# Performance work log

Measured on AMD Instinct MI355X. Metric: run time of the kernel, lower is better.

## Reference

```python
import jax, jax.numpy as jnp
import numpy as np

EPS = 1e-5
B, CIN, COUT, H, W = 32, 512, 512, 56, 56
K = 4            # kernel_num
A = 32           # attention_channel = max(int(512*0.0625), 16)


def setup_inputs() -> dict:
    key = jax.random.key(0)
    ks = jax.random.split(key, 16)
    s = lambda fan: 1.0 / np.sqrt(fan)
    return {
        "x": jax.random.normal(ks[0], (B, CIN, H, W), jnp.float32),
        # attention trunk: global-avgpool -> fc -> bn -> relu
        "fc_w": jax.random.normal(ks[1], (A, CIN), jnp.float32) * s(CIN),
        "abn_g": jnp.ones((A,), jnp.float32),
        "abn_b": jnp.zeros((A,), jnp.float32),
        "abn_m": jax.random.normal(ks[2], (A,), jnp.float32) * 0.1,
        "abn_v": jax.random.uniform(ks[3], (A,), jnp.float32, 0.5, 1.5),
        # channel / filter / kernel attention heads
        "ch_w": jax.random.normal(ks[4], (CIN, A), jnp.float32) * s(A),
        "ch_b": jnp.zeros((CIN,), jnp.float32),
        "fl_w": jax.random.normal(ks[5], (COUT, A), jnp.float32) * s(A),
        "fl_b": jnp.zeros((COUT,), jnp.float32),
        "kn_w": jax.random.normal(ks[6], (K, A), jnp.float32) * s(A),
        "kn_b": jnp.zeros((K,), jnp.float32),
        # base 1x1 conv weight bank [kernel_num, out, in] (1x1 spatial squeezed)
        "weight": jax.random.normal(ks[7], (K, COUT, CIN), jnp.float32) * s(CIN),
        # output BatchNorm2d (eval mode: running stats)
        "bn_g": jnp.ones((COUT,), jnp.float32),
        "bn_b": jnp.zeros((COUT,), jnp.float32),
        "bn_m": jax.random.normal(ks[8], (COUT,), jnp.float32) * 0.1,
        "bn_v": jax.random.uniform(ks[9], (COUT,), jnp.float32, 0.5, 1.5),
    }


def reference(x, fc_w, abn_g, abn_b, abn_m, abn_v,
              ch_w, ch_b, fl_w, fl_b, kn_w, kn_b,
              weight, bn_g, bn_b, bn_m, bn_v):
    # ---- omni-dimensional attention (kernel_size=1 => spatial attn skipped) ----
    pooled = jnp.mean(x, axis=(2, 3))                       # [B, Cin]
    h = pooled @ fc_w.T                                     # [B, A]
    h = (h - abn_m) * (abn_g / jnp.sqrt(abn_v + EPS)) + abn_b
    h = jax.nn.relu(h)
    ch_att = jax.nn.sigmoid(h @ ch_w.T + ch_b)              # [B, Cin]
    fl_att = jax.nn.sigmoid(h @ fl_w.T + fl_b)              # [B, Cout]
    kn_att = jax.nn.softmax(h @ kn_w.T + kn_b, axis=1)      # [B, K] (temperature=1)
    # ---- per-sample aggregated 1x1 kernel + grouped(batch) pointwise conv ----
    agg_w = jnp.einsum('bk,koc->boc', kn_att, weight)       # [B, Cout, Cin]
    xm = x * ch_att[:, :, None, None]                       # channel attention
    y = jnp.einsum('bchw,boc->bohw', xm, agg_w)             # batched 1x1 conv
    y = y * fl_att[:, :, None, None]                        # filter attention
    # ---- BatchNorm2d (inference) ----
    inv = bn_g / jnp.sqrt(bn_v + EPS)
    y = (y - bn_m[None, :, None, None]) * inv[None, :, None, None] + bn_b[None, :, None, None]
    return y
```

## Files before the change

### kernel.cpp

```cpp
#include <hip/hip_runtime.h>
#include <math.h>

#define BATCH 32
#define CIN   512
#define COUT  512
#define HW    3136
#define KNUM  4
#define ADIM  32
#define EPS   1e-5f

static constexpr size_t XT_OFF     = 0;
static constexpr size_t WF_OFF     = 102760448;
static constexpr size_t POOLED_OFF = 119537664;
static constexpr size_t H_OFF      = 119603200;
static constexpr size_t CH_OFF     = 119607296;
static constexpr size_t FLINV_OFF  = 119672832;
static constexpr size_t KN_OFF     = 119738368;
static constexpr size_t BETA_OFF   = 119738880;

typedef __attribute__((ext_vector_type(8))) short short8;
typedef __attribute__((ext_vector_type(4))) float float4v;

typedef const unsigned int __attribute__((address_space(1)))* gas_ptr;
typedef unsigned int __attribute__((address_space(3)))* lds_ptr;

__device__ __forceinline__ unsigned short f2bf(float f) {
  unsigned int u = __float_as_uint(f);
  u += 0x7FFFu + ((u >> 16) & 1u);
  return (unsigned short)(u >> 16);
}

__global__ void zero_f32(float* __restrict__ p, int n) {
  int i = blockIdx.x * blockDim.x + threadIdx.x;
  if (i < n) p[i] = 0.f;
}

__global__ __launch_bounds__(256) void transpose_pool(
    const float* __restrict__ x, unsigned short* __restrict__ xT,
    float* __restrict__ pooled) {
  __shared__ unsigned short T[64 * 68];
  const int pb = blockIdx.x * 64;
  const int cb = blockIdx.y * 64;
  const int b  = blockIdx.z;
  const int t  = threadIdx.x;
  const int mp = t & 15;
  const int mc = t >> 4;
  const int c0 = cb + mc * 4;
  const int p0 = pb + mp * 4;

  const float* xp = x + (size_t)(b * CIN + c0) * HW + p0;
  float a[4][4];
  #pragma unroll
  for (int r = 0; r < 4; ++r) {
    float4 v = *(const float4*)(xp + (size_t)r * HW);
    a[r][0] = v.x; a[r][1] = v.y; a[r][2] = v.z; a[r][3] = v.w;
    float s = v.x + v.y + v.z + v.w;
    #pragma unroll
    for (int off = 8; off > 0; off >>= 1) s += __shfl_down(s, off, 16);
    if (mp == 0) atomicAdd(&pooled[b * CIN + c0 + r], s);
  }
  #pragma unroll
  for (int j = 0; j < 4; ++j) {
    ushort4 w;
    w.x = f2bf(a[0][j]); w.y = f2bf(a[1][j]);
    w.z = f2bf(a[2][j]); w.w = f2bf(a[3][j]);
    *(ushort4*)&T[(mp * 4 + j) * 68 + mc * 4] = w;
  }
  __syncthreads();
  const int pr = t >> 2, cp = t & 3;
  const int base = pr * 68 + cp * 16;
  uint2 r0 = *(uint2*)&T[base + 0];
  uint2 r1 = *(uint2*)&T[base + 4];
  uint2 r2 = *(uint2*)&T[base + 8];
  uint2 r3 = *(uint2*)&T[base + 12];
  unsigned short* dst = xT + (size_t)(b * HW + pb + pr) * CIN + cb + cp * 16;
  *(uint4*)(dst)     = make_uint4(r0.x, r0.y, r1.x, r1.y);
  *(uint4*)(dst + 8) = make_uint4(r2.x, r2.y, r3.x, r3.y);
}

__global__ __launch_bounds__(256) void attn_h_kn(
    const float* __restrict__ pooled, const float* __restrict__ fc_w,
    const float* __restrict__ abn_g, const float* __restrict__ abn_b,
    const float* __restrict__ abn_m, const float* __restrict__ abn_v,
    const float* __restrict__ kn_w, const float* __restrict__ kn_b,
    float* __restrict__ h_out, float* __restrict__ kn_out) {
  __shared__ float hs[ADIM];
  const int b = blockIdx.x, t = threadIdx.x;
  const int a = t >> 3, part = t & 7;
  const float* pr = pooled + b * CIN;
  const float* fr = fc_w + a * CIN;
  float s = 0.f;
  const int cb = part * 64;
  #pragma unroll 8
  for (int c = 0; c < 64; ++c) s += pr[cb + c] * fr[cb + c];
  #pragma unroll
  for (int off = 4; off > 0; off >>= 1) s += __shfl_down(s, off, 8);
  if (part == 0) {
    s *= (1.0f / (float)HW);
    float vv = (s - abn_m[a]) * (abn_g[a] * rsqrtf(abn_v[a] + EPS)) + abn_b[a];
    vv = fmaxf(vv, 0.f);
    hs[a] = vv;
    h_out[b * ADIM + a] = vv;
  }
  __syncthreads();
  if (t == 0) {
    float lg[KNUM]; float mx = -1e30f;
    for (int k = 0; k < KNUM; ++k) {
      float acc = kn_b[k];
      for (int aa = 0; aa < ADIM; ++aa) acc += hs[aa] * kn_w[k * ADIM + aa];
      lg[k] = acc; mx = fmaxf(mx, acc);
    }
    float ssum = 0.f;
    for (int k = 0; k < KNUM; ++k) { lg[k] = expf(lg[k] - mx); ssum += lg[k]; }
    for (int k = 0; k < KNUM; ++k) kn_out[b * KNUM + k] = lg[k] / ssum;
  }
}

__global__ void beta_kernel(const float* __restrict__ bn_g, const float* __restrict__ bn_b,
                            const float* __restrict__ bn_m, const float* __restrict__ bn_v,
                            float* __restrict__ beta) {
  int o = blockIdx.x * 256 + threadIdx.x;
  if (o < COUT) {
    float inv = bn_g[o] * rsqrtf(bn_v[o] + EPS);
    beta[o] = bn_b[o] - bn_m[o] * inv;
  }
}

__global__ __launch_bounds__(128) void attn_heads(
    const float* __restrict__ h, const float* __restrict__ ch_w, const float* __restrict__ ch_b,
    const float* __restrict__ fl_w, const float* __restrict__ fl_b,
    const float* __restrict__ bn_g, const float* __restrict__ bn_v,
    float* __restrict__ ch_out, float* __restrict__ flinv_out) {
  __shared__ float hs[ADIM];
  const int ck = blockIdx.x, b = blockIdx.y, t = threadIdx.x;
  if (t < ADIM) hs[t] = h[b * ADIM + t];
  __syncthreads();
  if (ck < 4) {
    int c = ck * 128 + t;
    const float* wr = ch_w + c * ADIM;
    float acc = ch_b[c];
    #pragma unroll
    for (int aa = 0; aa < ADIM; ++aa) acc += hs[aa] * wr[aa];
    ch_out[b * CIN + c] = 1.f / (1.f + expf(-acc));
  } else {
    int o = (ck - 4) * 128 + t;
    const float* wr = fl_w + o * ADIM;
    float acc = fl_b[o];
    #pragma unroll
    for (int aa = 0; aa < ADIM; ++aa) acc += hs[aa] * wr[aa];
    float sig = 1.f / (1.f + expf(-acc));
    flinv_out[b * COUT + o] = sig * (bn_g[o] * rsqrtf(bn_v[o] + EPS));
  }
}

__global__ __launch_bounds__(256) void build_wf(
    const float* __restrict__ weight, const float* __restrict__ kn,
    const float* __restrict__ ch, const float* __restrict__ flinv,
    unsigned short* __restrict__ Wf) {
  const int och = blockIdx.x, b = blockIdx.y, t = threadIdx.x;
  const int o0 = och * 16;
  const float k0 = kn[b * KNUM + 0], k1 = kn[b * KNUM + 1];
  const float k2 = kn[b * KNUM + 2], k3 = kn[b * KNUM + 3];
  #pragma unroll
  for (int i = 0; i < 8; ++i) {
    int cell = i * 1024 + t * 4;
    int ol = cell >> 9, c = cell & 511;
    int o = o0 + ol;
    float fi = flinv[b * COUT + o];
    const float* wp = weight + (size_t)o * CIN + c;
    float4 w0 = *(const float4*)(wp);
    float4 w1 = *(const float4*)(wp + 1 * CIN * COUT);
    float4 w2 = *(const float4*)(wp + 2 * CIN * COUT);
    float4 w3 = *(const float4*)(wp + 3 * CIN * COUT);
    float4 cv = *(const float4*)(ch + b * CIN + c);
    ushort4 r;
    r.x = f2bf((k0 * w0.x + k1 * w1.x + k2 * w2.x + k3 * w3.x) * cv.x * fi);
    r.y = f2bf((k0 * w0.y + k1 * w1.y + k2 * w2.y + k3 * w3.y) * cv.y * fi);
    r.z = f2bf((k0 * w0.z + k1 * w1.z + k2 * w2.z + k3 * w3.z) * cv.z * fi);
    r.w = f2bf((k0 * w0.w + k1 * w1.w + k2 * w2.w + k3 * w3.w) * cv.w * fi);
    *(ushort4*)(Wf + (size_t)(b * COUT + o) * CIN + c) = r;
  }
}

__global__ __launch_bounds__(256) void gemm_kernel(
    const unsigned short* __restrict__ xT, const unsigned short* __restrict__ Wf,
    const float* __restrict__ beta, float* __restrict__ y) {
  __shared__ unsigned short lA[128 * 32];
  __shared__ unsigned short lB[128 * 32];
  const int pt = blockIdx.x, ot = blockIdx.y, b = blockIdx.z;
  const int o0 = ot * 128, p0 = pt * 128;
  const int t = threadIdx.x;
  const int wave = t >> 6, lane = t & 63;
  const int wm = wave & 1, wn = wave >> 1;

  const int lrow = lane >> 2;
  const int lcol = (lane & 3) * 8;
  const int r0 = (wave * 2 + 0) * 16 + lrow;
  const int r1 = (wave * 2 + 1) * 16 + lrow;

  const unsigned short* Ab = Wf + (size_t)b * COUT * CIN;
  const unsigned short* Bb = xT + (size_t)b * HW * CIN;
  const unsigned short* agp0 = Ab + (size_t)(o0 + r0) * CIN + lcol;
  const unsigned short* agp1 = Ab + (size_t)(o0 + r1) * CIN + lcol;
  int bp0 = p0 + r0; if (bp0 > HW - 1) bp0 = HW - 1;
  int bp1 = p0 + r1; if (bp1 > HW - 1) bp1 = HW - 1;
  const unsigned short* bgp0 = Bb + (size_t)bp0 * CIN + lcol;
  const unsigned short* bgp1 = Bb + (size_t)bp1 * CIN + lcol;

  unsigned short* lA0 = &lA[(wave * 2 + 0) * 512];
  unsigned short* lA1 = &lA[(wave * 2 + 1) * 512];
  unsigned short* lB0 = &lB[(wave * 2 + 0) * 512];
  unsigned short* lB1 = &lB[(wave * 2 + 1) * 512];

  float4v acc[4][4];
  #pragma unroll
  for (int i = 0; i < 4; ++i)
    #pragma unroll
    for (int j = 0; j < 4; ++j)
      #pragma unroll
      for (int r = 0; r < 4; ++r) acc[i][j][r] = 0.f;

  const int arow = lane & 15;
  const int kofs = (lane >> 4) * 8;

  for (int kt = 0; kt < CIN / 32; ++kt) {
    const int c0 = kt * 32;
    __syncthreads();
    __builtin_amdgcn_global_load_lds((gas_ptr)(const void*)(agp0 + c0), (lds_ptr)(void*)lA0, 16, 0, 0);
    __builtin_amdgcn_global_load_lds((gas_ptr)(const void*)(agp1 + c0), (lds_ptr)(void*)lA1, 16, 0, 0);
    __builtin_amdgcn_global_load_lds((gas_ptr)(const void*)(bgp0 + c0), (lds_ptr)(void*)lB0, 16, 0, 0);
    __builtin_amdgcn_global_load_lds((gas_ptr)(const void*)(bgp1 + c0), (lds_ptr)(void*)lB1, 16, 0, 0);
    __syncthreads();

    short8 af[4], bfr[4];
    #pragma unroll
    for (int i = 0; i < 4; ++i)
      af[i] = *(const short8*)&lA[(wm * 64 + i * 16 + arow) * 32 + kofs];
    #pragma unroll
    for (int j = 0; j < 4; ++j)
      bfr[j] = *(const short8*)&lB[(wn * 64 + j * 16 + arow) * 32 + kofs];
    #pragma unroll
    for (int i = 0; i < 4; ++i)
      #pragma unroll
      for (int j = 0; j < 4; ++j)
        acc[i][j] = __builtin_amdgcn_mfma_f32_16x16x32_bf16(af[i], bfr[j], acc[i][j], 0, 0, 0);
  }

  const int rowq = (lane >> 4) * 4;
  const int coln = lane & 15;
  #pragma unroll
  for (int i = 0; i < 4; ++i) {
    const int obase = o0 + wm * 64 + i * 16 + rowq;
    float bet[4];
    #pragma unroll
    for (int r = 0; r < 4; ++r) bet[r] = beta[obase + r];
    #pragma unroll
    for (int j = 0; j < 4; ++j) {
      const int p = p0 + wn * 64 + j * 16 + coln;
      if (p < HW) {
        #pragma unroll
        for (int r = 0; r < 4; ++r)
          y[(size_t)(b * COUT + obase + r) * HW + p] = acc[i][j][r] + bet[r];
      }
    }
  }
}

extern "C" void kernel_launch(void* const* d_in, const int* in_sizes, int n_in,
                              void* d_out, int out_size, void* d_ws, size_t ws_size,
                              hipStream_t stream) {
  (void)in_sizes; (void)n_in; (void)out_size; (void)ws_size;
  const float* x     = (const float*)d_in[0];
  const float* fc_w  = (const float*)d_in[1];
  const float* abn_g = (const float*)d_in[2];
  const float* abn_b = (const float*)d_in[3];
  const float* abn_m = (const float*)d_in[4];
  const float* abn_v = (const float*)d_in[5];
  const float* ch_w  = (const float*)d_in[6];
  const float* ch_b  = (const float*)d_in[7];
  const float* fl_w  = (const float*)d_in[8];
  const float* fl_b  = (const float*)d_in[9];
  const float* kn_w  = (const float*)d_in[10];
  const float* kn_b  = (const float*)d_in[11];
  const float* weight= (const float*)d_in[12];
  const float* bn_g  = (const float*)d_in[13];
  const float* bn_b  = (const float*)d_in[14];
  const float* bn_m  = (const float*)d_in[15];
  const float* bn_v  = (const float*)d_in[16];
  float* out = (float*)d_out;

  char* ws = (char*)d_ws;
  unsigned short* xT   = (unsigned short*)(ws + XT_OFF);
  unsigned short* Wf   = (unsigned short*)(ws + WF_OFF);
  float* pooled = (float*)(ws + POOLED_OFF);
  float* h      = (float*)(ws + H_OFF);
  float* ch     = (float*)(ws + CH_OFF);
  float* flinv  = (float*)(ws + FLINV_OFF);
  float* kn     = (float*)(ws + KN_OFF);
  float* beta   = (float*)(ws + BETA_OFF);

  zero_f32<<<64, 256, 0, stream>>>(pooled, BATCH * CIN);
  transpose_pool<<<dim3(HW / 64, CIN / 64, BATCH), 256, 0, stream>>>(x, xT, pooled);
  attn_h_kn<<<BATCH, 256, 0, stream>>>(pooled, fc_w, abn_g, abn_b, abn_m, abn_v,
                                       kn_w, kn_b, h, kn);
  beta_kernel<<<2, 256, 0, stream>>>(bn_g, bn_b, bn_m, bn_v, beta);
  attn_heads<<<dim3(8, BATCH), 128, 0, stream>>>(h, ch_w, ch_b, fl_w, fl_b, bn_g, bn_v,
                                                 ch, flinv);
  build_wf<<<dim3(32, BATCH), 256, 0, stream>>>(weight, kn, ch, flinv, Wf);
  gemm_kernel<<<dim3(25, 4, BATCH), 256, 0, stream>>>(xT, Wf, beta, out);
}
```

Measured before the change: 501.8 us.

## Fuse attention kernels, drop atomics, widen GEMM K-tile with swizzled LDS

Pooling no longer uses atomicAdd plus a zeroing kernel. Each transpose block now handles 256 channels and writes per-block partial sums, which a single fused attention kernel reduces before computing h, kernel, channel and filter attention. The separate beta kernel is gone and the BN bias is computed in the GEMM epilogue. The GEMM K-tile doubles to 64 with an XOR-swizzled LDS layout to avoid bank conflicts, halving loop iterations and barriers, and the grid order changes so the o-tiles sharing an xT tile run adjacently. The costs are more LDS per block and less parallelism in the transpose kernel.

```diff
diff --git a/kernel.cpp b/kernel.cpp
--- a/kernel.cpp
+++ b/kernel.cpp
@@ -9,14 +9,12 @@
 #define ADIM  32
 #define EPS   1e-5f
 
-static constexpr size_t XT_OFF     = 0;
-static constexpr size_t WF_OFF     = 102760448;
-static constexpr size_t POOLED_OFF = 119537664;
-static constexpr size_t H_OFF      = 119603200;
-static constexpr size_t CH_OFF     = 119607296;
-static constexpr size_t FLINV_OFF  = 119672832;
-static constexpr size_t KN_OFF     = 119738368;
-static constexpr size_t BETA_OFF   = 119738880;
+static constexpr size_t XT_OFF    = 0;
+static constexpr size_t WF_OFF    = 102760448;
+static constexpr size_t PART_OFF  = 119537664;
+static constexpr size_t CH_OFF    = 122748928;
+static constexpr size_t FLINV_OFF = 122814464;
+static constexpr size_t KN_OFF    = 122880000;
 
 typedef __attribute__((ext_vector_type(8))) short short8;
 typedef __attribute__((ext_vector_type(4))) float float4v;
@@ -30,77 +28,89 @@
   return (unsigned short)(u >> 16);
 }
 
-__global__ void zero_f32(float* __restrict__ p, int n) {
-  int i = blockIdx.x * blockDim.x + threadIdx.x;
-  if (i < n) p[i] = 0.f;
-}
-
 __global__ __launch_bounds__(256) void transpose_pool(
     const float* __restrict__ x, unsigned short* __restrict__ xT,
-    float* __restrict__ pooled) {
+    float* __restrict__ part) {
   __shared__ unsigned short T[64 * 68];
-  const int pb = blockIdx.x * 64;
-  const int cb = blockIdx.y * 64;
-  const int b  = blockIdx.z;
+  const int pb    = blockIdx.x * 64;
+  const int cbase = blockIdx.y * 256;
+  const int b     = blockIdx.z;
   const int t  = threadIdx.x;
   const int mp = t & 15;
   const int mc = t >> 4;
-  const int c0 = cb + mc * 4;
   const int p0 = pb + mp * 4;
-
-  const float* xp = x + (size_t)(b * CIN + c0) * HW + p0;
-  float a[4][4];
-  #pragma unroll
-  for (int r = 0; r < 4; ++r) {
-    float4 v = *(const float4*)(xp + (size_t)r * HW);
-    a[r][0] = v.x; a[r][1] = v.y; a[r][2] = v.z; a[r][3] = v.w;
-    float s = v.x + v.y + v.z + v.w;
-    #pragma unroll
-    for (int off = 8; off > 0; off >>= 1) s += __shfl_down(s, off, 16);
-    if (mp == 0) atomicAdd(&pooled[b * CIN + c0 + r], s);
-  }
-  #pragma unroll
-  for (int j = 0; j < 4; ++j) {
-    ushort4 w;
-    w.x = f2bf(a[0][j]); w.y = f2bf(a[1][j]);
-    w.z = f2bf(a[2][j]); w.w = f2bf(a[3][j]);
-    *(ushort4*)&T[(mp * 4 + j) * 68 + mc * 4] = w;
-  }
-  __syncthreads();
   const int pr = t >> 2, cp = t & 3;
-  const int base = pr * 68 + cp * 16;
-  uint2 r0 = *(uint2*)&T[base + 0];
-  uint2 r1 = *(uint2*)&T[base + 4];
-  uint2 r2 = *(uint2*)&T[base + 8];
-  uint2 r3 = *(uint2*)&T[base + 12];
-  unsigned short* dst = xT + (size_t)(b * HW + pb + pr) * CIN + cb + cp * 16;
-  *(uint4*)(dst)     = make_uint4(r0.x, r0.y, r1.x, r1.y);
-  *(uint4*)(dst + 8) = make_uint4(r2.x, r2.y, r3.x, r3.y);
-}
-
-__global__ __launch_bounds__(256) void attn_h_kn(
-    const float* __restrict__ pooled, const float* __restrict__ fc_w,
+
+  #pragma unroll
+  for (int sub = 0; sub < 4; ++sub) {
+    const int cb = cbase + sub * 64;
+    const int c0 = cb + mc * 4;
+    const float* xp = x + (size_t)(b * CIN + c0) * HW + p0;
+    float a[4][4];
+    #pragma unroll
+    for (int r = 0; r < 4; ++r) {
+      float4 v = *(const float4*)(xp + (size_t)r * HW);
+      a[r][0] = v.x; a[r][1] = v.y; a[r][2] = v.z; a[r][3] = v.w;
+      float s = v.x + v.y + v.z + v.w;
+      #pragma unroll
+      for (int off = 8; off > 0; off >>= 1) s += __shfl_down(s, off, 16);
+      if (mp == 0)
+        part[((size_t)b * 49 + blockIdx.x) * 512 + c0 + r] = s;
+    }
+    #pragma unroll
+    for (int j = 0; j < 4; ++j) {
+      ushort4 w;
+      w.x = f2bf(a[0][j]); w.y = f2bf(a[1][j]);
+      w.z = f2bf(a[2][j]); w.w = f2bf(a[3][j]);
+      *(ushort4*)&T[(mp * 4 + j) * 68 + mc * 4] = w;
+    }
+    __syncthreads();
+    const int base = pr * 68 + cp * 16;
+    uint2 r0 = *(uint2*)&T[base + 0];
+    uint2 r1 = *(uint2*)&T[base + 4];
+    uint2 r2 = *(uint2*)&T[base + 8];
+    uint2 r3 = *(uint2*)&T[base + 12];
+    unsigned short* dst = xT + (size_t)(b * HW + pb + pr) * CIN + cb + cp * 16;
+    *(uint4*)(dst)     = make_uint4(r0.x, r0.y, r1.x, r1.y);
+    *(uint4*)(dst + 8) = make_uint4(r2.x, r2.y, r3.x, r3.y);
+    __syncthreads();
+  }
+}
+
+__global__ __launch_bounds__(256) void attn_all(
+    const float* __restrict__ part, const float* __restrict__ fc_w,
     const float* __restrict__ abn_g, const float* __restrict__ abn_b,
     const float* __restrict__ abn_m, const float* __restrict__ abn_v,
     const float* __restrict__ kn_w, const float* __restrict__ kn_b,
-    float* __restrict__ h_out, float* __restrict__ kn_out) {
+    const float* __restrict__ ch_w, const float* __restrict__ ch_b,
+    const float* __restrict__ fl_w, const float* __restrict__ fl_b,
+    const float* __restrict__ bn_g, const float* __restrict__ bn_v,
+    float* __restrict__ ch_out, float* __restrict__ flinv_out,
+    float* __restrict__ kn_out) {
+  __shared__ float pooledS[CIN];
   __shared__ float hs[ADIM];
   const int b = blockIdx.x, t = threadIdx.x;
-  const int a = t >> 3, part = t & 7;
-  const float* pr = pooled + b * CIN;
-  const float* fr = fc_w + a * CIN;
-  float s = 0.f;
-  const int cb = part * 64;
-  #pragma unroll 8
-  for (int c = 0; c < 64; ++c) s += pr[cb + c] * fr[cb + c];
-  #pragma unroll
-  for (int off = 4; off > 0; off >>= 1) s += __shfl_down(s, off, 8);
-  if (part == 0) {
-    s *= (1.0f / (float)HW);
-    float vv = (s - abn_m[a]) * (abn_g[a] * rsqrtf(abn_v[a] + EPS)) + abn_b[a];
-    vv = fmaxf(vv, 0.f);
-    hs[a] = vv;
-    h_out[b * ADIM + a] = vv;
+  #pragma unroll
+  for (int idx = t; idx < CIN; idx += 256) {
+    float s = 0.f;
+    for (int j = 0; j < 49; ++j) s += part[((size_t)b * 49 + j) * 512 + idx];
+    pooledS[idx] = s;
+  }
+  __syncthreads();
+  {
+    const int a = t >> 3, pz = t & 7;
+    const float* fr = fc_w + a * CIN + pz * 64;
+    const float* pp = pooledS + pz * 64;
+    float s = 0.f;
+    #pragma unroll 8
+    for (int c = 0; c < 64; ++c) s += pp[c] * fr[c];
+    #pragma unroll
+    for (int off = 4; off > 0; off >>= 1) s += __shfl_down(s, off, 8);
+    if (pz == 0) {
+      s *= (1.0f / (float)HW);
+      float vv = (s - abn_m[a]) * (abn_g[a] * rsqrtf(abn_v[a] + EPS)) + abn_b[a];
+      hs[a] = fmaxf(vv, 0.f);
+    }
   }
   __syncthreads();
   if (t == 0) {
@@ -114,36 +124,16 @@
     for (int k = 0; k < KNUM; ++k) { lg[k] = expf(lg[k] - mx); ssum += lg[k]; }
     for (int k = 0; k < KNUM; ++k) kn_out[b * KNUM + k] = lg[k] / ssum;
   }
-}
-
-__global__ void beta_kernel(const float* __restrict__ bn_g, const float* __restrict__ bn_b,
-                            const float* __restrict__ bn_m, const float* __restrict__ bn_v,
-                            float* __restrict__ beta) {
-  int o = blockIdx.x * 256 + threadIdx.x;
-  if (o < COUT) {
-    float inv = bn_g[o] * rsqrtf(bn_v[o] + EPS);
-    beta[o] = bn_b[o] - bn_m[o] * inv;
-  }
-}
-
-__global__ __launch_bounds__(128) void attn_heads(
-    const float* __restrict__ h, const float* __restrict__ ch_w, const float* __restrict__ ch_b,
-    const float* __restrict__ fl_w, const float* __restrict__ fl_b,
-    const float* __restrict__ bn_g, const float* __restrict__ bn_v,
-    float* __restrict__ ch_out, float* __restrict__ flinv_out) {
-  __shared__ float hs[ADIM];
-  const int ck = blockIdx.x, b = blockIdx.y, t = threadIdx.x;
-  if (t < ADIM) hs[t] = h[b * ADIM + t];
-  __syncthreads();
-  if (ck < 4) {
-    int c = ck * 128 + t;
+  #pragma unroll
+  for (int c = t; c < CIN; c += 256) {
     const float* wr = ch_w + c * ADIM;
     float acc = ch_b[c];
     #pragma unroll
     for (int aa = 0; aa < ADIM; ++aa) acc += hs[aa] * wr[aa];
     ch_out[b * CIN + c] = 1.f / (1.f + expf(-acc));
-  } else {
-    int o = (ck - 4) * 128 + t;
+  }
+  #pragma unroll
+  for (int o = t; o < COUT; o += 256) {
     const float* wr = fl_w + o * ADIM;
     float acc = fl_b[o];
     #pragma unroll
@@ -182,35 +172,35 @@
   }
 }
 
-__global__ __launch_bounds__(256) void gemm_kernel(
+__global__ __launch_bounds__(256, 4) void gemm_kernel(
     const unsigned short* __restrict__ xT, const unsigned short* __restrict__ Wf,
-    const float* __restrict__ beta, float* __restrict__ y) {
-  __shared__ unsigned short lA[128 * 32];
-  __shared__ unsigned short lB[128 * 32];
-  const int pt = blockIdx.x, ot = blockIdx.y, b = blockIdx.z;
+    const float* __restrict__ bn_g, const float* __restrict__ bn_b,
+    const float* __restrict__ bn_m, const float* __restrict__ bn_v,
+    float* __restrict__ y) {
+  __shared__ unsigned short lA[128 * 64];
+  __shared__ unsigned short lB[128 * 64];
+  const int ot = blockIdx.x, pt = blockIdx.y, b = blockIdx.z;
   const int o0 = ot * 128, p0 = pt * 128;
   const int t = threadIdx.x;
   const int wave = t >> 6, lane = t & 63;
   const int wm = wave & 1, wn = wave >> 1;
 
-  const int lrow = lane >> 2;
-  const int lcol = (lane & 3) * 8;
-  const int r0 = (wave * 2 + 0) * 16 + lrow;
-  const int r1 = (wave * 2 + 1) * 16 + lrow;
+  const int srow = lane >> 3;
+  const int sgrp = lane & 7;
+  const int scol = ((sgrp ^ srow) * 8);
 
   const unsigned short* Ab = Wf + (size_t)b * COUT * CIN;
   const unsigned short* Bb = xT + (size_t)b * HW * CIN;
-  const unsigned short* agp0 = Ab + (size_t)(o0 + r0) * CIN + lcol;
-  const unsigned short* agp1 = Ab + (size_t)(o0 + r1) * CIN + lcol;
-  int bp0 = p0 + r0; if (bp0 > HW - 1) bp0 = HW - 1;
-  int bp1 = p0 + r1; if (bp1 > HW - 1) bp1 = HW - 1;
-  const unsigned short* bgp0 = Bb + (size_t)bp0 * CIN + lcol;
-  const unsigned short* bgp1 = Bb + (size_t)bp1 * CIN + lcol;
-
-  unsigned short* lA0 = &lA[(wave * 2 + 0) * 512];
-  unsigned short* lA1 = &lA[(wave * 2 + 1) * 512];
-  unsigned short* lB0 = &lB[(wave * 2 + 0) * 512];
-  unsigned short* lB1 = &lB[(wave * 2 + 1) * 512];
+  const unsigned short* aSrc[4];
+  const unsigned short* bSrc[4];
+  #pragma unroll
+  for (int q = 0; q < 4; ++q) {
+    const int ar = o0 + wave * 32 + q * 8 + srow;
+    aSrc[q] = Ab + (size_t)ar * CIN + scol;
+    int br = p0 + wave * 32 + q * 8 + srow;
+    if (br > HW - 1) br = HW - 1;
+    bSrc[q] = Bb + (size_t)br * CIN + scol;
+  }
 
   float4v acc[4][4];
   #pragma unroll
@@ -221,29 +211,38 @@
       for (int r = 0; r < 4; ++r) acc[i][j][r] = 0.f;
 
   const int arow = lane & 15;
-  const int kofs = (lane >> 4) * 8;
-
-  for (int kt = 0; kt < CIN / 32; ++kt) {
-    const int c0 = kt * 32;
+  const int kgrp = lane >> 4;
+  const int slot0 = ((0 + kgrp) ^ (arow & 7)) * 8;
+  const int slot1 = ((4 + kgrp) ^ (arow & 7)) * 8;
+
+  for (int kt = 0; kt < CIN / 64; ++kt) {
+    const int c0 = kt * 64;
     __syncthreads();
-    __builtin_amdgcn_global_load_lds((gas_ptr)(const void*)(agp0 + c0), (lds_ptr)(void*)lA0, 16, 0, 0);
-    __builtin_amdgcn_global_load_lds((gas_ptr)(const void*)(agp1 + c0), (lds_ptr)(void*)lA1, 16, 0, 0);
-    __builtin_amdgcn_global_load_lds((gas_ptr)(const void*)(bgp0 + c0), (lds_ptr)(void*)lB0, 16, 0, 0);
-    __builtin_amdgcn_global_load_lds((gas_ptr)(const void*)(bgp1 + c0), (lds_ptr)(void*)lB1, 16, 0, 0);
+    #pragma unroll
+    for (int q = 0; q < 4; ++q) {
+      __builtin_amdgcn_global_load_lds((gas_ptr)(const void*)(aSrc[q] + c0),
+          (lds_ptr)(void*)&lA[(wave * 32 + q * 8) * 64], 16, 0, 0);
+      __builtin_amdgcn_global_load_lds((gas_ptr)(const void*)(bSrc[q] + c0),
+          (lds_ptr)(void*)&lB[(wave * 32 + q * 8) * 64], 16, 0, 0);
+    }
     __syncthreads();
 
-    short8 af[4], bfr[4];
-    #pragma unroll
-    for (int i = 0; i < 4; ++i)
-      af[i] = *(const short8*)&lA[(wm * 64 + i * 16 + arow) * 32 + kofs];
-    #pragma unroll
-    for (int j = 0; j < 4; ++j)
-      bfr[j] = *(const short8*)&lB[(wn * 64 + j * 16 + arow) * 32 + kofs];
-    #pragma unroll
-    for (int i = 0; i < 4; ++i)
+    #pragma unroll
+    for (int ks = 0; ks < 2; ++ks) {
+      const int sl = ks ? slot1 : slot0;
+      short8 af[4], bfr[4];
+      #pragma unroll
+      for (int i = 0; i < 4; ++i)
+        af[i] = *(const short8*)&lA[(wm * 64 + i * 16 + arow) * 64 + sl];
       #pragma unroll
       for (int j = 0; j < 4; ++j)
-        acc[i][j] = __builtin_amdgcn_mfma_f32_16x16x32_bf16(af[i], bfr[j], acc[i][j], 0, 0, 0);
+        bfr[j] = *(const short8*)&lB[(wn * 64 + j * 16 + arow) * 64 + sl];
+      #pragma unroll
+      for (int i = 0; i < 4; ++i)
+        #pragma unroll
+        for (int j = 0; j < 4; ++j)
+          acc[i][j] = __builtin_amdgcn_mfma_f32_16x16x32_bf16(af[i], bfr[j], acc[i][j], 0, 0, 0);
+    }
   }
 
   const int rowq = (lane >> 4) * 4;
@@ -253,7 +252,11 @@
     const int obase = o0 + wm * 64 + i * 16 + rowq;
     float bet[4];
     #pragma unroll
-    for (int r = 0; r < 4; ++r) bet[r] = beta[obase + r];
+    for (int r = 0; r < 4; ++r) {
+      const int o = obase + r;
+      const float inv = bn_g[o] * rsqrtf(bn_v[o] + EPS);
+      bet[r] = bn_b[o] - bn_m[o] * inv;
+    }
     #pragma unroll
     for (int j = 0; j < 4; ++j) {
       const int p = p0 + wn * 64 + j * 16 + coln;
@@ -290,22 +293,17 @@
   float* out = (float*)d_out;
 
   char* ws = (char*)d_ws;
-  unsigned short* xT   = (unsigned short*)(ws + XT_OFF);
-  unsigned short* Wf   = (unsigned short*)(ws + WF_OFF);
-  float* pooled = (float*)(ws + POOLED_OFF);
-  float* h      = (float*)(ws + H_OFF);
-  float* ch     = (float*)(ws + CH_OFF);
-  float* flinv  = (float*)(ws + FLINV_OFF);
-  float* kn     = (float*)(ws + KN_OFF);
-  float* beta   = (float*)(ws + BETA_OFF);
-
-  zero_f32<<<64, 256, 0, stream>>>(pooled, BATCH * CIN);
-  transpose_pool<<<dim3(HW / 64, CIN / 64, BATCH), 256, 0, stream>>>(x, xT, pooled);
-  attn_h_kn<<<BATCH, 256, 0, stream>>>(pooled, fc_w, abn_g, abn_b, abn_m, abn_v,
-                                       kn_w, kn_b, h, kn);
-  beta_kernel<<<2, 256, 0, stream>>>(bn_g, bn_b, bn_m, bn_v, beta);
-  attn_heads<<<dim3(8, BATCH), 128, 0, stream>>>(h, ch_w, ch_b, fl_w, fl_b, bn_g, bn_v,
-                                                 ch, flinv);
+  unsigned short* xT = (unsigned short*)(ws + XT_OFF);
+  unsigned short* Wf = (unsigned short*)(ws + WF_OFF);
+  float* part  = (float*)(ws + PART_OFF);
+  float* ch    = (float*)(ws + CH_OFF);
+  float* flinv = (float*)(ws + FLINV_OFF);
+  float* kn    = (float*)(ws + KN_OFF);
+
+  transpose_pool<<<dim3(49, 2, BATCH), 256, 0, stream>>>(x, xT, part);
+  attn_all<<<BATCH, 256, 0, stream>>>(part, fc_w, abn_g, abn_b, abn_m, abn_v,
+                                      kn_w, kn_b, ch_w, ch_b, fl_w, fl_b,
+                                      bn_g, bn_v, ch, flinv, kn);
   build_wf<<<dim3(32, BATCH), 256, 0, stream>>>(weight, kn, ch, flinv, Wf);
-  gemm_kernel<<<dim3(25, 4, BATCH), 256, 0, stream>>>(xT, Wf, beta, out);
-}
+  gemm_kernel<<<dim3(4, 25, BATCH), 256, 0, stream>>>(xT, Wf, bn_g, bn_b, bn_m, bn_v, out);
+}
```

New measurement: 498.1 us. Within noise of the previous version (-0.7%).
